# Kernel tuning notes

Hardware: AMD Instinct MI355X
Metric: run time of the kernel (lower is better)

The kernel has to match this reference:

```python
import jax, jax.numpy as jnp
import numpy as np

B, T, E, H = 4, 2048, 1024, 16
HD = E // H  # 64


def setup_inputs() -> dict:
    key = jax.random.key(0)
    ks = jax.random.split(key, 7)
    s = 0.02
    return {
        "values": jax.random.normal(ks[0], (B, T, E), jnp.float32),
        "keys": jax.random.normal(ks[1], (B, T, E), jnp.float32),
        "query": jax.random.normal(ks[2], (B, T, E), jnp.float32),
        "Wv": jax.random.normal(ks[3], (HD, HD), jnp.float32) * s,
        "Wk": jax.random.normal(ks[4], (HD, HD), jnp.float32) * s,
        "Wq": jax.random.normal(ks[5], (HD, HD), jnp.float32) * s,
        "Wo": jax.random.normal(ks[6], (E, E), jnp.float32) * s,
    }


def _proj_split(x, W):
    # x: [B,T,E] -> per-head projection with shared [HD,HD] weight -> [B,H,T,HD]
    xh = x.reshape(B, T, H, HD)
    return jnp.einsum("bthd,ed->bhte", xh, W)  # torch Linear: x @ W.T


def reference(values, keys, query, Wv, Wk, Wq, Wo):
    v = _proj_split(values, Wv)   # [B,H,T,HD]
    k = _proj_split(keys, Wk)
    q = _proj_split(query, Wq)
    scale = 1.0 / np.sqrt(HD).astype(np.float32)
    scores = jnp.einsum("bhqd,bhkd->bhqk", q, k) * scale  # [B,H,T,T]
    probs = jax.nn.softmax(scores, axis=-1)
    attn = jnp.einsum("bhqk,bhkd->bhqd", probs, v)        # [B,H,T,HD]
    out = attn.transpose(0, 2, 1, 3).reshape(B, T, E)      # combine heads
    return out @ Wo.T
```

## Files before the change

kernel.cpp:

```cpp
#include <hip/hip_runtime.h>


typedef __bf16 bf16x8 __attribute__((ext_vector_type(8)));
typedef float f32x4 __attribute__((ext_vector_type(4)));
typedef float f32x16 __attribute__((ext_vector_type(16)));
typedef unsigned int u32x2v __attribute__((ext_vector_type(2)));
typedef unsigned int u32x4v __attribute__((ext_vector_type(4)));

#define DEVI static __device__ __forceinline__

constexpr int Bc = 4, Tc = 2048, Ec = 1024, HDc = 64;
constexpr int BHc = 64;

DEVI unsigned short f2bf(float f) {
  unsigned int u = __builtin_bit_cast(unsigned int, f);
  u += 0x7fffu + ((u >> 16) & 1u);
  return (unsigned short)(u >> 16);
}

DEVI int swzf(int row) { return (row & 7) ^ ((row >> 3) & 3); }

DEVI bf16x8 lds_frag(const unsigned short* base, int row, int chunk) {
  const char* p = reinterpret_cast<const char*>(base) + row * 128 + ((chunk ^ swzf(row)) * 16);
  return *reinterpret_cast<const bf16x8*>(p);
}
DEVI void lds_store16(unsigned short* base, int row, int ci, uint4 v) {
  char* p = reinterpret_cast<char*>(base) + row * 128 + ((ci ^ swzf(row)) * 16);
  *reinterpret_cast<uint4*>(p) = v;
}
DEVI uint4 pack8(float4 a, float4 b) {
  uint4 o;
  o.x = f2bf(a.x) | ((unsigned)f2bf(a.y) << 16);
  o.y = f2bf(a.z) | ((unsigned)f2bf(a.w) << 16);
  o.z = f2bf(b.x) | ((unsigned)f2bf(b.y) << 16);
  o.w = f2bf(b.z) | ((unsigned)f2bf(b.w) << 16);
  return o;
}

DEVI unsigned cvt_pk_bf16(float lo, float hi) {
  unsigned r;
  asm("v_cvt_pk_bf16_f32 %0, %1, %2" : "=v"(r) : "v"(lo), "v"(hi));
  return r;
}
DEVI float exp2_fast(float x) {
  float r;
  asm("v_exp_f32 %0, %1" : "=v"(r) : "v"(x));
  return r;
}
DEVI void plswap(unsigned& a, unsigned& b) {
#if __has_builtin(__builtin_amdgcn_permlane32_swap)
  u32x2v r = __builtin_amdgcn_permlane32_swap(a, b, false, false);
  a = r.x; b = r.y;
#else
  int lane = threadIdx.x & 63;
  unsigned sa = (unsigned)__shfl_xor((int)a, 32), sb = (unsigned)__shfl_xor((int)b, 32);
  unsigned na = (lane < 32) ? a : sb;
  unsigned nb = (lane < 32) ? sa : b;
  a = na; b = nb;
#endif
}
DEVI float halfsum(float x) {
  unsigned a = __builtin_bit_cast(unsigned, x), b = a;
  plswap(a, b);
  return __builtin_bit_cast(float, a) + __builtin_bit_cast(float, b);
}

DEVI void gload16(const unsigned short* g, unsigned short* l) {
  __builtin_amdgcn_global_load_lds(
      (const __attribute__((address_space(1))) void*)g,
      (__attribute__((address_space(3))) void*)l, 16, 0, 0);
}

__global__ __launch_bounds__(256) void proj3_kernel(
    const float* __restrict__ xv, const float* __restrict__ xk,
    const float* __restrict__ xq, const float* __restrict__ Wv,
    const float* __restrict__ Wk, const float* __restrict__ Wq,
    unsigned short* __restrict__ ov, unsigned short* __restrict__ ok,
    unsigned short* __restrict__ oq, float qscale) {
  const int which = blockIdx.z;
  const float* x = which == 0 ? xv : which == 1 ? xk : xq;
  const float* W = which == 0 ? Wv : which == 1 ? Wk : Wq;
  unsigned short* out = which == 0 ? ov : which == 1 ? ok : oq;
  const int transposed = (which == 0);
  const float wscale = (which == 2) ? qscale : 1.0f;

  __shared__ __align__(16) unsigned short Xl[64 * 64];
  __shared__ __align__(16) unsigned short Wl[64 * 64];
  const int tid = threadIdx.x;
  const int bh = blockIdx.y, t0 = blockIdx.x * 64;
  const int b = bh >> 4, h = bh & 15;
  const float* xbase = x + (size_t)(b * Tc + t0) * Ec + h * HDc;

#pragma unroll
  for (int it = 0; it < 2; ++it) {
    int ch = tid + it * 256;
    int row = ch >> 3, ci = ch & 7;
    float4 wa = *reinterpret_cast<const float4*>(W + row * 64 + ci * 8);
    float4 wb = *reinterpret_cast<const float4*>(W + row * 64 + ci * 8 + 4);
    wa.x *= wscale; wa.y *= wscale; wa.z *= wscale; wa.w *= wscale;
    wb.x *= wscale; wb.y *= wscale; wb.z *= wscale; wb.w *= wscale;
    lds_store16(Wl, row, ci, pack8(wa, wb));
    float4 xa = *reinterpret_cast<const float4*>(xbase + (size_t)row * Ec + ci * 8);
    float4 xb = *reinterpret_cast<const float4*>(xbase + (size_t)row * Ec + ci * 8 + 4);
    lds_store16(Xl, row, ci, pack8(xa, xb));
  }
  __syncthreads();

  const int lane = tid & 63, wv = tid >> 6;
  const int c16 = lane & 15, hi = lane >> 4;
  f32x4 acc[4];
#pragma unroll
  for (int nb = 0; nb < 4; ++nb) acc[nb] = {0.f, 0.f, 0.f, 0.f};
  if (!transposed) {
#pragma unroll
    for (int c = 0; c < 2; ++c) {
      bf16x8 aX = lds_frag(Xl, 16 * wv + c16, 4 * c + hi);
#pragma unroll
      for (int nb = 0; nb < 4; ++nb) {
        bf16x8 bW = lds_frag(Wl, 16 * nb + c16, 4 * c + hi);
        acc[nb] = __builtin_amdgcn_mfma_f32_16x16x32_bf16(aX, bW, acc[nb], 0, 0, 0);
      }
    }
#pragma unroll
    for (int nb = 0; nb < 4; ++nb)
#pragma unroll
      for (int r = 0; r < 4; ++r) {
        int t = t0 + 16 * wv + 4 * hi + r;
        int e = 16 * nb + c16;
        out[(size_t)(bh * Tc + t) * HDc + e] = f2bf(acc[nb][r]);
      }
  } else {
#pragma unroll
    for (int c = 0; c < 2; ++c) {
      bf16x8 aW = lds_frag(Wl, 16 * wv + c16, 4 * c + hi);
#pragma unroll
      for (int nb = 0; nb < 4; ++nb) {
        bf16x8 bX = lds_frag(Xl, 16 * nb + c16, 4 * c + hi);
        acc[nb] = __builtin_amdgcn_mfma_f32_16x16x32_bf16(aW, bX, acc[nb], 0, 0, 0);
      }
    }
#pragma unroll
    for (int nb = 0; nb < 4; ++nb)
#pragma unroll
      for (int r = 0; r < 4; ++r) {
        int e = 16 * wv + 4 * hi + r;
        int t = t0 + 16 * nb + c16;
        out[(size_t)(bh * HDc + e) * Tc + t] = f2bf(acc[nb][r]);
      }
  }
}

__global__ __launch_bounds__(256) void cast_wo(const float* __restrict__ Wsrc,
                                               unsigned short* __restrict__ dst) {
  size_t i = (size_t)blockIdx.x * 256 + threadIdx.x;
  float4 f = *reinterpret_cast<const float4*>(Wsrc + i * 4);
  uint2 o;
  o.x = f2bf(f.x) | ((unsigned)f2bf(f.y) << 16);
  o.y = f2bf(f.z) | ((unsigned)f2bf(f.w) << 16);
  *reinterpret_cast<uint2*>(dst + i * 4) = o;
}

DEVI void stage_kv(const unsigned short* __restrict__ Kp,
                   const unsigned short* __restrict__ Vp, int kt,
                   unsigned short* Kl, unsigned short* Vl, int wv, int lane) {
#pragma unroll
  for (int j = 0; j < 2; ++j) {
    const int base = (4 * j + wv) * 64;
    const int slot = base + lane;
    const int row = slot >> 3;
    const int sc = ((slot & 7) ^ swzf(row)) * 8;
    gload16(Kp + (size_t)(kt * 64 + row) * 64 + sc, Kl + base * 8);
    gload16(Vp + (size_t)row * Tc + kt * 64 + sc, Vl + base * 8);
  }
}

DEVI float exp_sum_pf(f32x16& s0, f32x16& s1, bf16x8 pf[4]) {
#pragma unroll
  for (int i = 0; i < 16; ++i) s0[i] = exp2_fast(s0[i]);
#pragma unroll
  for (int i = 0; i < 16; ++i) s1[i] = exp2_fast(s1[i]);
  float t[16];
#pragma unroll
  for (int i = 0; i < 16; ++i) t[i] = s0[i] + s1[i];
#pragma unroll
  for (int i = 0; i < 8; ++i) t[i] += t[i + 8];
#pragma unroll
  for (int i = 0; i < 4; ++i) t[i] += t[i + 4];
  float rs = (t[0] + t[1]) + (t[2] + t[3]);
  unsigned w0[8], w1[8];
#pragma unroll
  for (int i = 0; i < 8; ++i) w0[i] = cvt_pk_bf16(s0[2 * i], s0[2 * i + 1]);
#pragma unroll
  for (int i = 0; i < 8; ++i) w1[i] = cvt_pk_bf16(s1[2 * i], s1[2 * i + 1]);
  plswap(w0[0], w0[2]); plswap(w0[1], w0[3]); plswap(w0[4], w0[6]); plswap(w0[5], w0[7]);
  plswap(w1[0], w1[2]); plswap(w1[1], w1[3]); plswap(w1[4], w1[6]); plswap(w1[5], w1[7]);
  pf[0] = __builtin_bit_cast(bf16x8, (u32x4v){w0[0], w0[1], w0[2], w0[3]});
  pf[1] = __builtin_bit_cast(bf16x8, (u32x4v){w0[4], w0[5], w0[6], w0[7]});
  pf[2] = __builtin_bit_cast(bf16x8, (u32x4v){w1[0], w1[1], w1[2], w1[3]});
  pf[3] = __builtin_bit_cast(bf16x8, (u32x4v){w1[4], w1[5], w1[6], w1[7]});
  return rs;
}

__global__ __launch_bounds__(256, 2) void attn_kernel(
    const unsigned short* __restrict__ Qb_, const unsigned short* __restrict__ Kb_,
    const unsigned short* __restrict__ Vtb_, unsigned short* __restrict__ O) {
  __shared__ __align__(16) unsigned short KV[4][2][64 * 64];
  const int tid = threadIdx.x, lane = tid & 63, wv = tid >> 6;
  const int c32 = lane & 31, hi = lane >> 5;
  const int flat = blockIdx.y * (int)gridDim.x + blockIdx.x;
  const int logical = (flat & 7) * 64 + (flat >> 3);
  const int q0 = (logical & 7) * 256, bh = logical >> 3;
  const int b = bh >> 4, h = bh & 15;
  const unsigned short* Qp = Qb_ + (size_t)bh * Tc * HDc;
  const unsigned short* Kp = Kb_ + (size_t)bh * Tc * HDc;
  const unsigned short* Vp = Vtb_ + (size_t)bh * HDc * Tc;

  const int tA = q0 + 64 * wv + c32, tB = tA + 32;
  bf16x8 qfA[4], qfB[4];
#pragma unroll
  for (int c = 0; c < 4; ++c) {
    qfA[c] = *reinterpret_cast<const bf16x8*>(Qp + (size_t)tA * HDc + 16 * c + 8 * hi);
    qfB[c] = *reinterpret_cast<const bf16x8*>(Qp + (size_t)tB * HDc + 16 * c + 8 * hi);
  }

  stage_kv(Kp, Vp, 0, KV[0][0], KV[0][1], wv, lane);
  stage_kv(Kp, Vp, 1, KV[1][0], KV[1][1], wv, lane);

  f32x16 aA0, aA1, aB0, aB1, zv;
#pragma unroll
  for (int i = 0; i < 16; ++i) {
    aA0[i] = 0.f; aA1[i] = 0.f; aB0[i] = 0.f; aB1[i] = 0.f; zv[i] = 0.f;
  }
  float lA = 0.f, lB = 0.f;

  auto qk2 = [&](const unsigned short* Kl, f32x16& sA0, f32x16& sA1,
                 f32x16& sB0, f32x16& sB1) {
    __builtin_amdgcn_s_setprio(1);
    {
      bf16x8 k0 = lds_frag(Kl, c32, hi);
      sA0 = __builtin_amdgcn_mfma_f32_32x32x16_bf16(k0, qfA[0], zv, 0, 0, 0);
      sB0 = __builtin_amdgcn_mfma_f32_32x32x16_bf16(k0, qfB[0], zv, 0, 0, 0);
      bf16x8 k1 = lds_frag(Kl, 32 + c32, hi);
      sA1 = __builtin_amdgcn_mfma_f32_32x32x16_bf16(k1, qfA[0], zv, 0, 0, 0);
      sB1 = __builtin_amdgcn_mfma_f32_32x32x16_bf16(k1, qfB[0], zv, 0, 0, 0);
    }
#pragma unroll
    for (int c = 1; c < 4; ++c) {
      bf16x8 k0 = lds_frag(Kl, c32, 2 * c + hi);
      sA0 = __builtin_amdgcn_mfma_f32_32x32x16_bf16(k0, qfA[c], sA0, 0, 0, 0);
      sB0 = __builtin_amdgcn_mfma_f32_32x32x16_bf16(k0, qfB[c], sB0, 0, 0, 0);
      bf16x8 k1 = lds_frag(Kl, 32 + c32, 2 * c + hi);
      sA1 = __builtin_amdgcn_mfma_f32_32x32x16_bf16(k1, qfA[c], sA1, 0, 0, 0);
      sB1 = __builtin_amdgcn_mfma_f32_32x32x16_bf16(k1, qfB[c], sB1, 0, 0, 0);
    }
    __builtin_amdgcn_s_setprio(0);
  };
  auto pv2 = [&](const unsigned short* Vl, bf16x8 pfA[4], bf16x8 pfB[4]) {
    __builtin_amdgcn_s_setprio(1);
#pragma unroll
    for (int ks = 0; ks < 4; ++ks) {
      bf16x8 v0 = lds_frag(Vl, c32, 2 * ks + hi);
      aA0 = __builtin_amdgcn_mfma_f32_32x32x16_bf16(v0, pfA[ks], aA0, 0, 0, 0);
      aB0 = __builtin_amdgcn_mfma_f32_32x32x16_bf16(v0, pfB[ks], aB0, 0, 0, 0);
      bf16x8 v1 = lds_frag(Vl, 32 + c32, 2 * ks + hi);
      aA1 = __builtin_amdgcn_mfma_f32_32x32x16_bf16(v1, pfA[ks], aA1, 0, 0, 0);
      aB1 = __builtin_amdgcn_mfma_f32_32x32x16_bf16(v1, pfB[ks], aB1, 0, 0, 0);
    }
    __builtin_amdgcn_s_setprio(0);
  };

  constexpr int NT = Tc / 64;
  f32x16 sA0, sA1, sB0, sB1;

  asm volatile("s_waitcnt vmcnt(4)" ::: "memory");
  __builtin_amdgcn_s_barrier();
  qk2(KV[0][0], sA0, sA1, sB0, sB1);

  for (int t = 0; t < NT; ++t) {
    if (t + 2 < NT) {
      stage_kv(Kp, Vp, t + 2, KV[(t + 2) & 3][0], KV[(t + 2) & 3][1], wv, lane);
      asm volatile("s_waitcnt vmcnt(4)" ::: "memory");
    } else if (t + 1 < NT) {
      asm volatile("s_waitcnt vmcnt(0)" ::: "memory");
    }
    __builtin_amdgcn_s_barrier();
    bf16x8 pfA[4], pfB[4];
    lA += exp_sum_pf(sA0, sA1, pfA);
    lB += exp_sum_pf(sB0, sB1, pfB);
    if (t + 1 < NT) qk2(KV[(t + 1) & 3][0], sA0, sA1, sB0, sB1);
    pv2(KV[t & 3][1], pfA, pfB);
  }

  {
    const float rl = 1.0f / halfsum(lA);
    unsigned short* orow = O + (size_t)(b * Tc + tA) * Ec + h * HDc;
#pragma unroll
    for (int rq = 0; rq < 4; ++rq) {
      uint2 p0, p1;
      p0.x = cvt_pk_bf16(aA0[4 * rq] * rl, aA0[4 * rq + 1] * rl);
      p0.y = cvt_pk_bf16(aA0[4 * rq + 2] * rl, aA0[4 * rq + 3] * rl);
      *reinterpret_cast<uint2*>(orow + 8 * rq + 4 * hi) = p0;
      p1.x = cvt_pk_bf16(aA1[4 * rq] * rl, aA1[4 * rq + 1] * rl);
      p1.y = cvt_pk_bf16(aA1[4 * rq + 2] * rl, aA1[4 * rq + 3] * rl);
      *reinterpret_cast<uint2*>(orow + 32 + 8 * rq + 4 * hi) = p1;
    }
  }
  {
    const float rl = 1.0f / halfsum(lB);
    unsigned short* orow = O + (size_t)(b * Tc + tB) * Ec + h * HDc;
#pragma unroll
    for (int rq = 0; rq < 4; ++rq) {
      uint2 p0, p1;
      p0.x = cvt_pk_bf16(aB0[4 * rq] * rl, aB0[4 * rq + 1] * rl);
      p0.y = cvt_pk_bf16(aB0[4 * rq + 2] * rl, aB0[4 * rq + 3] * rl);
      *reinterpret_cast<uint2*>(orow + 8 * rq + 4 * hi) = p0;
      p1.x = cvt_pk_bf16(aB1[4 * rq] * rl, aB1[4 * rq + 1] * rl);
      p1.y = cvt_pk_bf16(aB1[4 * rq + 2] * rl, aB1[4 * rq + 3] * rl);
      *reinterpret_cast<uint2*>(orow + 32 + 8 * rq + 4 * hi) = p1;
    }
  }
}

DEVI void stage_ab(const unsigned short* __restrict__ Ap,
                   const unsigned short* __restrict__ Bp, int kt,
                   unsigned short* Al, unsigned short* Bl, int wv, int lane) {
#pragma unroll
  for (int j = 0; j < 4; ++j) {
    const int base = (4 * j + wv) * 64;
    const int slot = base + lane;
    const int row = slot >> 3;
    const int sc = ((slot & 7) ^ swzf(row)) * 8;
    gload16(Ap + (size_t)row * Ec + kt * 64 + sc, Al + base * 8);
    gload16(Bp + (size_t)row * Ec + kt * 64 + sc, Bl + base * 8);
  }
}

__global__ __launch_bounds__(256, 2) void ogemm_kernel(
    const unsigned short* __restrict__ A, const unsigned short* __restrict__ Bw,
    float* __restrict__ out) {
  __shared__ __align__(16) unsigned short Al[2][128 * 64];
  __shared__ __align__(16) unsigned short Bl[2][128 * 64];
  const int tid = threadIdx.x, lane = tid & 63, wv = tid >> 6;
  const int c32 = lane & 31, hi = lane >> 5;
  const int flat = blockIdx.y * (int)gridDim.x + blockIdx.x;
  const int logical = (flat & 7) * 64 + (flat >> 3);
  const int n0 = (logical & 7) * 128, m0 = (logical >> 3) * 128;
  const int wr = wv >> 1, wc = wv & 1;
  const unsigned short* Ap = A + (size_t)m0 * Ec;
  const unsigned short* Bp = Bw + (size_t)n0 * Ec;

  f32x16 acc[2][2];
#pragma unroll
  for (int mi = 0; mi < 2; ++mi)
#pragma unroll
    for (int ni = 0; ni < 2; ++ni)
#pragma unroll
      for (int i = 0; i < 16; ++i) acc[mi][ni][i] = 0.f;

  auto gtile = [&](const unsigned short* Alc, const unsigned short* Blc) {
    __builtin_amdgcn_s_setprio(1);
#pragma unroll
    for (int kc = 0; kc < 4; ++kc) {
      bf16x8 x0 = lds_frag(Alc, 64 * wr + c32, 2 * kc + hi);
      bf16x8 x1 = lds_frag(Alc, 64 * wr + 32 + c32, 2 * kc + hi);
      bf16x8 y0 = lds_frag(Blc, 64 * wc + c32, 2 * kc + hi);
      bf16x8 y1 = lds_frag(Blc, 64 * wc + 32 + c32, 2 * kc + hi);
      acc[0][0] = __builtin_amdgcn_mfma_f32_32x32x16_bf16(x0, y0, acc[0][0], 0, 0, 0);
      acc[0][1] = __builtin_amdgcn_mfma_f32_32x32x16_bf16(x0, y1, acc[0][1], 0, 0, 0);
      acc[1][0] = __builtin_amdgcn_mfma_f32_32x32x16_bf16(x1, y0, acc[1][0], 0, 0, 0);
      acc[1][1] = __builtin_amdgcn_mfma_f32_32x32x16_bf16(x1, y1, acc[1][1], 0, 0, 0);
    }
    __builtin_amdgcn_s_setprio(0);
  };

  stage_ab(Ap, Bp, 0, Al[0], Bl[0], wv, lane);
  __syncthreads();
  for (int kt = 0; kt < Ec / 64; kt += 2) {
    stage_ab(Ap, Bp, kt + 1, Al[1], Bl[1], wv, lane);
    gtile(Al[0], Bl[0]);
    __syncthreads();
    if (kt + 2 < Ec / 64) stage_ab(Ap, Bp, kt + 2, Al[0], Bl[0], wv, lane);
    gtile(Al[1], Bl[1]);
    __syncthreads();
  }

  const int nb = n0 + 64 * wc + c32;
  const int mb = m0 + 64 * wr + 4 * hi;
#pragma unroll
  for (int mi = 0; mi < 2; ++mi)
#pragma unroll
    for (int ni = 0; ni < 2; ++ni)
#pragma unroll
      for (int rq = 0; rq < 4; ++rq)
#pragma unroll
        for (int j = 0; j < 4; ++j) {
          int mrow = mb + 32 * mi + 8 * rq + j;
          out[(size_t)mrow * Ec + nb + 32 * ni] = acc[mi][ni][4 * rq + j];
        }
}

extern "C" void kernel_launch(void* const* d_in, const int* in_sizes, int n_in,
                              void* d_out, int out_size, void* d_ws, size_t ws_size,
                              hipStream_t stream) {
  (void)in_sizes; (void)n_in; (void)out_size; (void)ws_size;
  const float* values = (const float*)d_in[0];
  const float* keys   = (const float*)d_in[1];
  const float* query  = (const float*)d_in[2];
  const float* Wv = (const float*)d_in[3];
  const float* Wk = (const float*)d_in[4];
  const float* Wq = (const float*)d_in[5];
  const float* Wo = (const float*)d_in[6];
  float* out = (float*)d_out;

  char* ws = (char*)d_ws;
  constexpr size_t SZ = (size_t)BHc * Tc * HDc * 2;
  unsigned short* qb  = (unsigned short*)(ws + 0 * SZ);
  unsigned short* kb  = (unsigned short*)(ws + 1 * SZ);
  unsigned short* vt  = (unsigned short*)(ws + 2 * SZ);
  unsigned short* at  = (unsigned short*)(ws + 3 * SZ);
  unsigned short* wob = (unsigned short*)(ws + 4 * SZ);

  dim3 blk(256);
  proj3_kernel<<<dim3(Tc / 64, BHc, 3), blk, 0, stream>>>(
      values, keys, query, Wv, Wk, Wq, vt, kb, qb, 0.18033688011112042f);
  cast_wo<<<dim3(Ec * Ec / 1024), blk, 0, stream>>>(Wo, wob);
  attn_kernel<<<dim3(Tc / 256, BHc), blk, 0, stream>>>(qb, kb, vt, at);
  ogemm_kernel<<<dim3(Ec / 128, (Bc * Tc) / 128), blk, 0, stream>>>(at, wob, out);
}
```

Baseline: 126.7 us.

## Stagger odd waves' PV behind softmax and fold Wo cast into projection launch

Odd-indexed waves in the attention loop now run the PV product for the previous tile before doing the exp/softmax and next QK, while even waves keep the original order. Waves on a SIMD then alternate between MFMA and exp work instead of all contending for the same unit at once. Because odd waves read V one tile later, the V buffer ring grows from 4 to 5 slots, which adds LDS. Separately, the Wo bf16 cast moves into an extra z-slice of the projection kernel, removing one kernel launch at the cost of many idle blocks in that slice.

```diff
diff --git a/kernel.cpp b/kernel.cpp
--- a/kernel.cpp
+++ b/kernel.cpp
@@ -75,8 +75,21 @@
     const float* __restrict__ xv, const float* __restrict__ xk,
     const float* __restrict__ xq, const float* __restrict__ Wv,
     const float* __restrict__ Wk, const float* __restrict__ Wq,
-    unsigned short* __restrict__ ov, unsigned short* __restrict__ ok,
-    unsigned short* __restrict__ oq, float qscale) {
+    const float* __restrict__ Wo, unsigned short* __restrict__ ov,
+    unsigned short* __restrict__ ok, unsigned short* __restrict__ oq,
+    unsigned short* __restrict__ wob, float qscale) {
+  if (blockIdx.z == 3) {
+    int cb = blockIdx.y * (int)gridDim.x + blockIdx.x;
+    if (cb < 1024) {
+      size_t i = (size_t)cb * 1024 + (size_t)threadIdx.x * 4;
+      float4 f = *reinterpret_cast<const float4*>(Wo + i);
+      uint2 o;
+      o.x = f2bf(f.x) | ((unsigned)f2bf(f.y) << 16);
+      o.y = f2bf(f.z) | ((unsigned)f2bf(f.w) << 16);
+      *reinterpret_cast<uint2*>(wob + i) = o;
+    }
+    return;
+  }
   const int which = blockIdx.z;
   const float* x = which == 0 ? xv : which == 1 ? xk : xq;
   const float* W = which == 0 ? Wv : which == 1 ? Wk : Wq;
@@ -150,16 +163,6 @@
   }
 }
 
-__global__ __launch_bounds__(256) void cast_wo(const float* __restrict__ Wsrc,
-                                               unsigned short* __restrict__ dst) {
-  size_t i = (size_t)blockIdx.x * 256 + threadIdx.x;
-  float4 f = *reinterpret_cast<const float4*>(Wsrc + i * 4);
-  uint2 o;
-  o.x = f2bf(f.x) | ((unsigned)f2bf(f.y) << 16);
-  o.y = f2bf(f.z) | ((unsigned)f2bf(f.w) << 16);
-  *reinterpret_cast<uint2*>(dst + i * 4) = o;
-}
-
 DEVI void stage_kv(const unsigned short* __restrict__ Kp,
                    const unsigned short* __restrict__ Vp, int kt,
                    unsigned short* Kl, unsigned short* Vl, int wv, int lane) {
@@ -204,7 +207,8 @@
 __global__ __launch_bounds__(256, 2) void attn_kernel(
     const unsigned short* __restrict__ Qb_, const unsigned short* __restrict__ Kb_,
     const unsigned short* __restrict__ Vtb_, unsigned short* __restrict__ O) {
-  __shared__ __align__(16) unsigned short KV[4][2][64 * 64];
+  __shared__ __align__(16) unsigned short Kbuf[4][64 * 64];
+  __shared__ __align__(16) unsigned short Vbuf[5][64 * 64];
   const int tid = threadIdx.x, lane = tid & 63, wv = tid >> 6;
   const int c32 = lane & 31, hi = lane >> 5;
   const int flat = blockIdx.y * (int)gridDim.x + blockIdx.x;
@@ -223,8 +227,8 @@
     qfB[c] = *reinterpret_cast<const bf16x8*>(Qp + (size_t)tB * HDc + 16 * c + 8 * hi);
   }
 
-  stage_kv(Kp, Vp, 0, KV[0][0], KV[0][1], wv, lane);
-  stage_kv(Kp, Vp, 1, KV[1][0], KV[1][1], wv, lane);
+  stage_kv(Kp, Vp, 0, Kbuf[0], Vbuf[0], wv, lane);
+  stage_kv(Kp, Vp, 1, Kbuf[1], Vbuf[1], wv, lane);
 
   f32x16 aA0, aA1, aB0, aB1, zv;
 #pragma unroll
@@ -271,25 +275,34 @@
 
   constexpr int NT = Tc / 64;
   f32x16 sA0, sA1, sB0, sB1;
+  bf16x8 pfA[4], pfB[4];
+  const bool oddw = (wv & 1);
 
   asm volatile("s_waitcnt vmcnt(4)" ::: "memory");
   __builtin_amdgcn_s_barrier();
-  qk2(KV[0][0], sA0, sA1, sB0, sB1);
+  qk2(Kbuf[0], sA0, sA1, sB0, sB1);
 
   for (int t = 0; t < NT; ++t) {
     if (t + 2 < NT) {
-      stage_kv(Kp, Vp, t + 2, KV[(t + 2) & 3][0], KV[(t + 2) & 3][1], wv, lane);
+      stage_kv(Kp, Vp, t + 2, Kbuf[(t + 2) & 3], Vbuf[(t + 2) % 5], wv, lane);
       asm volatile("s_waitcnt vmcnt(4)" ::: "memory");
     } else if (t + 1 < NT) {
       asm volatile("s_waitcnt vmcnt(0)" ::: "memory");
     }
     __builtin_amdgcn_s_barrier();
-    bf16x8 pfA[4], pfB[4];
-    lA += exp_sum_pf(sA0, sA1, pfA);
-    lB += exp_sum_pf(sB0, sB1, pfB);
-    if (t + 1 < NT) qk2(KV[(t + 1) & 3][0], sA0, sA1, sB0, sB1);
-    pv2(KV[t & 3][1], pfA, pfB);
-  }
+    if (!oddw) {
+      lA += exp_sum_pf(sA0, sA1, pfA);
+      lB += exp_sum_pf(sB0, sB1, pfB);
+      if (t + 1 < NT) qk2(Kbuf[(t + 1) & 3], sA0, sA1, sB0, sB1);
+      pv2(Vbuf[t % 5], pfA, pfB);
+    } else {
+      if (t > 0) pv2(Vbuf[(t + 4) % 5], pfA, pfB);
+      lA += exp_sum_pf(sA0, sA1, pfA);
+      lB += exp_sum_pf(sB0, sB1, pfB);
+      if (t + 1 < NT) qk2(Kbuf[(t + 1) & 3], sA0, sA1, sB0, sB1);
+    }
+  }
+  if (oddw) pv2(Vbuf[(NT - 1) % 5], pfA, pfB);
 
   {
     const float rl = 1.0f / halfsum(lA);
@@ -421,9 +434,9 @@
   unsigned short* wob = (unsigned short*)(ws + 4 * SZ);
 
   dim3 blk(256);
-  proj3_kernel<<<dim3(Tc / 64, BHc, 3), blk, 0, stream>>>(
-      values, keys, query, Wv, Wk, Wq, vt, kb, qb, 0.18033688011112042f);
-  cast_wo<<<dim3(Ec * Ec / 1024), blk, 0, stream>>>(Wo, wob);
+  proj3_kernel<<<dim3(Tc / 64, BHc, 4), blk, 0, stream>>>(
+      values, keys, query, Wv, Wk, Wq, Wo, vt, kb, qb, wob,
+      0.18033688011112042f);
   attn_kernel<<<dim3(Tc / 256, BHc), blk, 0, stream>>>(qb, kb, vt, at);
   ogemm_kernel<<<dim3(Ec / 128, (Bc * Tc) / 128), blk, 0, stream>>>(at, wob, out);
 }
```

Result: slower. 293.1 us (+131.3%).
